# Performance work log

Measured on AMD Instinct MI355X. Metric: run time of the kernel, lower is better.

Reference implementation:

```python
import jax, jax.numpy as jnp
import numpy as np

B, N_ATOMS = 64, 127            # graphs, atoms per graph (uniform)
L = N_ATOMS + 1                 # +1 cls token
D_MODEL, NHEAD, NUM_LAYERS, D_FF = 1024, 16, 8, 3072
HEAD_DIM = D_MODEL // NHEAD
MAX_TOKENS = 131                # 121 + 10
NEIGH_VOCAB = 14 + 3            # max_neighbors + 3
DIST_VOCAB = 83 + 3             # max_distance + 3
EPS = 1e-5


def _dist_bins():
    # short_cutoff=0.9, long_cutoff=5.0, precision=0.05; first 3 edges overridden
    b = np.arange(0.9 - 3 * 0.05, 5.0, 0.05)
    b[:3] = [-1.0, 0.0, 0.01]
    return jnp.asarray(b, jnp.float32)  # len 85 -> digitize indices in [0, 85]


def _layer_norm(x, g, b):
    m = jnp.mean(x, -1, keepdims=True)
    v = jnp.var(x, -1, keepdims=True)
    return (x - m) * jax.lax.rsqrt(v + EPS) * g + b


def setup_inputs() -> dict:
    key = jax.random.key(0)
    ks = jax.random.split(key, 16)
    s = 0.02
    z = jax.random.randint(ks[0], (B * N_ATOMS,), 0, 119)
    hgs = jax.random.randint(ks[1], (B * N_ATOMS,), 0, 15)
    pos = jax.random.normal(ks[2], (B * N_ATOMS, 3), jnp.float32) * 3.0
    batch = jnp.repeat(jnp.arange(B, dtype=jnp.int64), N_ATOMS)
    atoms_emb = (jax.random.normal(ks[3], (MAX_TOKENS, D_MODEL), jnp.float32) * s).at[0].set(0.0)  # padding_idx=0
    neigh_emb = (jax.random.normal(ks[4], (NEIGH_VOCAB, D_MODEL), jnp.float32) * s).at[0].set(0.0)
    dist_emb = jax.random.normal(ks[5], (DIST_VOCAB, NHEAD), jnp.float32) * s  # row 0 forced to -inf in reference
    Wqkv = jax.random.normal(ks[6], (D_MODEL, 3 * D_MODEL), jnp.float32) * s
    bqkv = jnp.zeros((3 * D_MODEL,), jnp.float32)
    Wo = jax.random.normal(ks[7], (D_MODEL, D_MODEL), jnp.float32) * s
    bo = jnp.zeros((D_MODEL,), jnp.float32)
    W1 = jax.random.normal(ks[8], (D_MODEL, D_FF), jnp.float32) * s
    b1f = jnp.zeros((D_FF,), jnp.float32)
    W2 = jax.random.normal(ks[9], (D_FF, D_MODEL), jnp.float32) * s
    b2f = jnp.zeros((D_MODEL,), jnp.float32)
    ln1_g = jnp.ones((D_MODEL,), jnp.float32); ln1_b = jnp.zeros((D_MODEL,), jnp.float32)
    ln2_g = jnp.ones((D_MODEL,), jnp.float32); ln2_b = jnp.zeros((D_MODEL,), jnp.float32)
    return dict(z=z, hgs=hgs, pos=pos, batch=batch, atoms_emb=atoms_emb, neigh_emb=neigh_emb,
                dist_emb=dist_emb, Wqkv=Wqkv, bqkv=bqkv, Wo=Wo, bo=bo,
                W1=W1, b1f=b1f, W2=W2, b2f=b2f,
                ln1_g=ln1_g, ln1_b=ln1_b, ln2_g=ln2_g, ln2_b=ln2_b)


def reference(z, hgs, pos, batch, atoms_emb, neigh_emb, dist_emb,
              Wqkv, bqkv, Wo, bo, W1, b1f, W2, b2f, ln1_g, ln1_b, ln2_g, ln2_b):
    # batch is uniform (N_ATOMS per graph, sorted), so per-graph batching == reshape
    zb = z.reshape(B, N_ATOMS).astype(jnp.int32) + 2
    hb = hgs.reshape(B, N_ATOMS).astype(jnp.int32) + 2
    atoms = jnp.concatenate([jnp.ones((B, 1), jnp.int32), zb], axis=1)        # cls token = 1
    neighbors = jnp.concatenate([jnp.zeros((B, 1), jnp.int32), hb], axis=1)   # cls neighbors = 0

    p = pos.reshape(B, N_ATOMS, 3)
    dist = jnp.sqrt(jnp.sum((p[:, None, :, :] - p[:, :, None, :]) ** 2, axis=-1))  # (B,n,n)
    didx = jnp.digitize(dist, _dist_bins()).astype(jnp.int32)                      # self-loop -> 2
    distances = jnp.ones((B, L, L), jnp.int32).at[:, 1:, 1:].set(didx)             # cls row/col = 1

    # neg_inf_idx=0 padding mask row (unused here since no padding -> indices >= 1)
    w_d = dist_emb.at[0].set(-jnp.inf)
    d_mask = w_d[distances].transpose(0, 3, 1, 2)  # (B, H, L, L)

    x = atoms_emb[atoms] + neigh_emb[neighbors]    # (B, L, D)
    scale = 1.0 / jnp.sqrt(jnp.float32(HEAD_DIM))
    for _ in range(NUM_LAYERS):  # shared weights + shared attention bias
        qkv = x @ Wqkv + bqkv
        q, k, v = jnp.split(qkv, 3, axis=-1)
        q = q.reshape(B, L, NHEAD, HEAD_DIM)
        k = k.reshape(B, L, NHEAD, HEAD_DIM)
        v = v.reshape(B, L, NHEAD, HEAD_DIM)
        scores = jnp.einsum('blhd,bmhd->bhlm', q, k) * scale + d_mask
        a = jax.nn.softmax(scores, axis=-1)
        o = jnp.einsum('bhlm,bmhd->blhd', a, v).reshape(B, L, D_MODEL) @ Wo + bo
        x = _layer_norm(x + o, ln1_g, ln1_b)                      # post-norm (norm_first=False)
        h = jax.nn.gelu(x @ W1 + b1f, approximate=False) @ W2 + b2f
        x = _layer_norm(x + h, ln2_g, ln2_b)
    return x[:, 0]  # cls embedding, (B, D_MODEL)
```

## Files before the change

kernel.cpp:

```cpp
#include <hip/hip_runtime.h>
#include <cstdint>
#include <math.h>

typedef unsigned short u16;
typedef __attribute__((ext_vector_type(4))) float f32x4;
typedef __attribute__((ext_vector_type(8))) __bf16 bf16x8;
typedef __attribute__((ext_vector_type(8))) short short8;

typedef __attribute__((address_space(1))) void g_void;
typedef __attribute__((address_space(3))) void l_void;

__device__ __forceinline__ u16 f2bf(float f) {
  uint32_t u = __builtin_bit_cast(uint32_t, f);
  u += 0x7FFFu + ((u >> 16) & 1u);
  return (u16)(u >> 16);
}
__device__ __forceinline__ float bf2f(u16 h) {
  uint32_t u = ((uint32_t)h) << 16;
  return __builtin_bit_cast(float, u);
}

__device__ __forceinline__ void gload16(const void* g, void* l) {
  __builtin_amdgcn_global_load_lds((g_void*)g, (l_void*)l, 16, 0, 0);
}

__device__ __forceinline__ float gelu_exact(float x) {
  float a = x * 0.70710678118654752f;
  float s = fabsf(a);
  float t = __builtin_amdgcn_rcpf(fmaf(0.3275911f, s, 1.0f));
  float p = fmaf(fmaf(fmaf(fmaf(1.061405429f, t, -1.453152027f), t, 1.421413741f), t,
                      -0.284496736f), t, 0.254829592f);
  p *= t;
  float e = __expf(-s * s);
  float er = fmaf(-p, e, 1.0f);
  er = copysignf(er, a);
  return 0.5f * x * (1.0f + er);
}

__global__ void transpose_w(const float* __restrict__ W, u16* __restrict__ Wt, int K, int N) {
  __shared__ float t[32][33];
  const int nb = blockIdx.x * 32, kb = blockIdx.y * 32;
  const int tx = threadIdx.x, ty = threadIdx.y;
#pragma unroll
  for (int i = 0; i < 32; i += 8)
    t[ty + i][tx] = W[(size_t)(kb + ty + i) * N + nb + tx];
  __syncthreads();
#pragma unroll
  for (int i = 0; i < 32; i += 8)
    Wt[(size_t)(nb + ty + i) * K + kb + tx] = f2bf(t[tx][ty + i]);
}

__global__ void embed_k(const int* __restrict__ z, const int* __restrict__ hgs,
                        const float* __restrict__ ae, const float* __restrict__ ne,
                        u16* __restrict__ xb) {
  const int row = blockIdx.x;
  const int b = row >> 7, tl = row & 127;
  int ia = 1, in_ = 0;
  if (tl > 0) { ia = z[b * 127 + tl - 1] + 2; in_ = hgs[b * 127 + tl - 1] + 2; }
  const float* ar = ae + (size_t)ia * 1024;
  const float* nr = ne + (size_t)in_ * 1024;
  for (int c = threadIdx.x; c < 1024; c += 256)
    xb[(size_t)row * 1024 + c] = f2bf(ar[c] + nr[c]);
}

__global__ void mask_k(const float* __restrict__ pos, const float* __restrict__ demb,
                       u16* __restrict__ mask) {
  __shared__ float edges[85];
  __shared__ float dhT[16 * 86];
  const int blk = blockIdx.x;
  const int b = blk >> 7, lk = blk & 127;
  const int lq = threadIdx.x;
  if (lq < 85) {
    double e = 0.75 + 0.05 * (double)lq;
    float ef = (float)e;
    if (lq == 0) ef = -1.0f; else if (lq == 1) ef = 0.0f; else if (lq == 2) ef = 0.01f;
    edges[lq] = ef;
  }
  for (int i = lq; i < 16 * 86; i += 128) {
    const int h = i / 86, c = i - h * 86;
    float v = (c == 0) ? -INFINITY : demb[c * 16 + h] * 8.0f;
    dhT[i] = v;
  }
  __syncthreads();
  int c;
  if (lq == 0 || lk == 0) {
    c = 1;
  } else {
    const float* pi = pos + ((size_t)b * 127 + lq - 1) * 3;
    const float* pj = pos + ((size_t)b * 127 + lk - 1) * 3;
    const float dx = pi[0] - pj[0], dy = pi[1] - pj[1], dz = pi[2] - pj[2];
    const float d = sqrtf(dx * dx + dy * dy + dz * dz);
    int cnt = 0;
#pragma unroll
    for (int k2 = 0; k2 < 85; ++k2) cnt += (edges[k2] <= d) ? 1 : 0;
    c = cnt;
  }
#pragma unroll
  for (int h = 0; h < 16; ++h)
    mask[((size_t)(b * 16 + h) << 14) + lk * 128 + lq] = f2bf(dhT[h * 86 + c]);
}

template <int MODE>
__launch_bounds__(512, 4)
__global__ void gemmS(const u16* __restrict__ A, const u16* __restrict__ Bt,
                      const float* __restrict__ bias,
                      u16* __restrict__ O0, u16* __restrict__ O1, u16* __restrict__ O2,
                      int N, int K) {
  extern __shared__ char lds[];
  constexpr int SLAB = 24576;
  const int tid = threadIdx.x;
  const int w = tid >> 6, l = tid & 63;
  const int wr = w >> 1, wc = w & 1;
  const int nwg = gridDim.x;
  const int wg = (blockIdx.x & 7) * (nwg >> 3) + (blockIdx.x >> 3);
  const int ntn = N >> 7;
  const int bm = wg / ntn, bn = wg - (wg / ntn) * ntn;
  const int NT = K >> 5;

  const int colc = ((((l & 3) << 4) ^ (((l >> 2) & 8) << 2)) >> 1);
  const u16* Ag = A + (size_t)(bm * 256 + w * 16 + (l >> 2)) * K + colc;
  const u16* Bg = Bt + (size_t)(bn * 128 + w * 16 + (l >> 2)) * K + colc;
  const int ldst = w << 10;

  const int lo = ((l & 15) << 6) + (((l >> 4) << 4) ^ ((l & 8) << 2));

  f32x4 acc[4][4];
#pragma unroll
  for (int m = 0; m < 4; ++m)
#pragma unroll
    for (int n = 0; n < 4; ++n) acc[m][n] = f32x4{0.f, 0.f, 0.f, 0.f};

  char* p0 = lds;
  char* p1 = lds + SLAB;
  char* p2 = lds + 2 * SLAB;

  {
    gload16(Ag + 0, p0 + ldst);
    gload16(Ag + (size_t)128 * K + 0, p0 + 8192 + ldst);
    gload16(Bg + 0, p0 + 16384 + ldst);
    gload16(Ag + 32, p1 + ldst);
    gload16(Ag + (size_t)128 * K + 32, p1 + 8192 + ldst);
    gload16(Bg + 32, p1 + 16384 + ldst);
  }
  asm volatile("s_waitcnt vmcnt(3)" ::: "memory");
  __builtin_amdgcn_s_barrier();

  for (int t = 0; t < NT; ++t) {
    const bool pre = (t + 2 < NT);
    const int kb2 = (t + 2) << 5;
    const char* ab = p0 + (wr << 12);
    const char* bb = p0 + 16384 + (wc << 12);
    bf16x8 af[4], bf[4];
#pragma unroll
    for (int m = 0; m < 4; ++m) af[m] = *(const bf16x8*)(ab + (m << 10) + lo);
#pragma unroll
    for (int n = 0; n < 2; ++n) bf[n] = *(const bf16x8*)(bb + (n << 10) + lo);
    if (pre) {
      gload16(Ag + kb2, p2 + ldst);
      gload16(Ag + (size_t)128 * K + kb2, p2 + 8192 + ldst);
    }
    __builtin_amdgcn_s_barrier();
    asm volatile("s_waitcnt lgkmcnt(0)" ::: "memory");
    __builtin_amdgcn_s_setprio(1);
#pragma unroll
    for (int m = 0; m < 4; ++m)
#pragma unroll
      for (int n = 0; n < 2; ++n)
        acc[m][n] = __builtin_amdgcn_mfma_f32_16x16x32_bf16(af[m], bf[n], acc[m][n], 0, 0, 0);
    __builtin_amdgcn_s_setprio(0);
    __builtin_amdgcn_s_barrier();
#pragma unroll
    for (int n = 2; n < 4; ++n) bf[n] = *(const bf16x8*)(bb + (n << 10) + lo);
    if (pre) gload16(Bg + kb2, p2 + 16384 + ldst);
    __builtin_amdgcn_s_barrier();
    asm volatile("s_waitcnt lgkmcnt(0)" ::: "memory");
    __builtin_amdgcn_s_setprio(1);
#pragma unroll
    for (int m = 0; m < 4; ++m)
#pragma unroll
      for (int n = 2; n < 4; ++n)
        acc[m][n] = __builtin_amdgcn_mfma_f32_16x16x32_bf16(af[m], bf[n], acc[m][n], 0, 0, 0);
    __builtin_amdgcn_s_setprio(0);
    if (pre) asm volatile("s_waitcnt vmcnt(3)" ::: "memory");
    else     asm volatile("s_waitcnt vmcnt(0)" ::: "memory");
    __builtin_amdgcn_s_barrier();
    char* tmp = p0; p0 = p1; p1 = p2; p2 = tmp;
  }

  const int fr = l & 15, fq = l >> 4;
  const int colb = bn * 128 + wc * 64;
  const int rowb = bm * 256 + wr * 64;
  float bv[4];
#pragma unroll
  for (int n = 0; n < 4; ++n) bv[n] = bias[colb + n * 16 + fr];
  const int region = colb >> 10;

#pragma unroll
  for (int m = 0; m < 4; ++m) {
#pragma unroll
    for (int n = 0; n < 4; ++n) {
      const int col = colb + n * 16 + fr;
      if (MODE == 0 && region == 2) {
        const int row0_ = rowb + m * 16 + fq * 4;
        const int bI = row0_ >> 7, tl0 = row0_ & 127;
        const int c = col & 1023, h = c >> 6, d = c & 63;
        ushort4 pk;
        pk.x = f2bf(acc[m][n][0] + bv[n]);
        pk.y = f2bf(acc[m][n][1] + bv[n]);
        pk.z = f2bf(acc[m][n][2] + bv[n]);
        pk.w = f2bf(acc[m][n][3] + bv[n]);
        *(ushort4*)&O2[(((size_t)bI * 16 + h) * 64 + d) * 128 + tl0] = pk;
      } else {
#pragma unroll
        for (int j = 0; j < 4; ++j) {
          const int row = rowb + m * 16 + fq * 4 + j;
          float v = acc[m][n][j] + bv[n];
          if (MODE == 2) v = gelu_exact(v);
          if (MODE == 0) {
            const int bI = row >> 7, tl = row & 127;
            const int c = col & 1023, h = c >> 6, d = c & 63;
            if (region == 0) O0[(((size_t)bI * 16 + h) * 128 + tl) * 64 + d] = f2bf(v);
            else             O1[(((size_t)bI * 16 + h) * 128 + tl) * 64 + d] = f2bf(v);
          } else {
            O0[(size_t)row * N + col] = f2bf(v);
          }
        }
      }
    }
  }
}

__launch_bounds__(256, 2)
__global__ void gemm4r(const u16* __restrict__ A, const u16* __restrict__ Bt,
                       const float* __restrict__ bias, u16* __restrict__ O,
                       int N, int K) {
  extern __shared__ char lds[];
  const int tid = threadIdx.x;
  const int w = tid >> 6, l = tid & 63;
  const int wr = w >> 1, wc = w & 1;
  const int nwg = gridDim.x;
  const int wg = (blockIdx.x & 7) * (nwg >> 3) + (blockIdx.x >> 3);
  const int ntn = N >> 7;
  const int bm = wg / ntn, bn = wg - (wg / ntn) * ntn;
  const int NT = K >> 5;

  const int colc = ((((l & 3) << 4) ^ (((l >> 2) & 8) << 2)) >> 1);
  const u16* Ag = A + (size_t)(bm * 128 + w * 16 + (l >> 2)) * K + colc;
  const u16* Bg = Bt + (size_t)(bn * 128 + w * 16 + (l >> 2)) * K + colc;
  const int ldst = w << 10;

  auto stage = [&](int t) {
    char* buf = lds + ((t & 3) << 14);
    const int kb = t << 5;
    gload16(Ag + kb, buf + ldst);
    gload16(Ag + (size_t)64 * K + kb, buf + 4096 + ldst);
    gload16(Bg + kb, buf + 8192 + ldst);
    gload16(Bg + (size_t)64 * K + kb, buf + 12288 + ldst);
  };

  const int lo = ((l & 15) << 6) + (((l >> 4) << 4) ^ ((l & 8) << 2));

  f32x4 acc[4][4];
#pragma unroll
  for (int m = 0; m < 4; ++m)
#pragma unroll
    for (int n = 0; n < 4; ++n) acc[m][n] = f32x4{0.f, 0.f, 0.f, 0.f};

  auto compute = [&](int bi) {
    const char* ab = lds + (bi << 14) + (wr << 12);
    const char* bb = lds + (bi << 14) + 8192 + (wc << 12);
    bf16x8 af[4], bf[4];
#pragma unroll
    for (int m = 0; m < 4; ++m) af[m] = *(const bf16x8*)(ab + (m << 10) + lo);
#pragma unroll
    for (int n = 0; n < 4; ++n) bf[n] = *(const bf16x8*)(bb + (n << 10) + lo);
    __builtin_amdgcn_s_setprio(1);
#pragma unroll
    for (int m = 0; m < 4; ++m)
#pragma unroll
      for (int n = 0; n < 4; ++n)
        acc[m][n] = __builtin_amdgcn_mfma_f32_16x16x32_bf16(af[m], bf[n], acc[m][n], 0, 0, 0);
    __builtin_amdgcn_s_setprio(0);
  };

  stage(0); stage(1); stage(2);
  asm volatile("s_waitcnt vmcnt(8)" ::: "memory");
  __builtin_amdgcn_s_barrier();

  for (int t4 = 0; t4 + 4 < NT; t4 += 4) {
#pragma unroll
    for (int u = 0; u < 4; ++u) {
      stage(t4 + u + 3);
      compute(u);
      asm volatile("s_waitcnt vmcnt(8)" ::: "memory");
      __builtin_amdgcn_s_barrier();
    }
  }
  stage(NT - 1);
  compute(0);
  asm volatile("s_waitcnt vmcnt(8)" ::: "memory");
  __builtin_amdgcn_s_barrier();
  compute(1);
  asm volatile("s_waitcnt vmcnt(4)" ::: "memory");
  __builtin_amdgcn_s_barrier();
  compute(2);
  asm volatile("s_waitcnt vmcnt(0)" ::: "memory");
  __builtin_amdgcn_s_barrier();
  compute(3);

  const int fr = l & 15, fq = l >> 4;
  const int colb = bn * 128 + wc * 64;
  const int rowb = bm * 128 + wr * 64;
  float bv[4];
#pragma unroll
  for (int n = 0; n < 4; ++n) bv[n] = bias[colb + n * 16 + fr];
#pragma unroll
  for (int m = 0; m < 4; ++m)
#pragma unroll
    for (int n = 0; n < 4; ++n) {
      const int col = colb + n * 16 + fr;
#pragma unroll
      for (int j = 0; j < 4; ++j) {
        const int row = rowb + m * 16 + fq * 4 + j;
        O[(size_t)row * N + col] = f2bf(acc[m][n][j] + bv[n]);
      }
    }
}

__launch_bounds__(256)
__global__ void attn_kernel(const u16* __restrict__ Qg, const u16* __restrict__ Kg,
                            const u16* __restrict__ Vg,
                            const u16* __restrict__ mask,
                            u16* __restrict__ Og) {
  __shared__ u16 QK[2 * 128 * 64];
  __shared__ u16 Vt[64 * 128];
  const int tid = threadIdx.x;
  const int wv = tid >> 6;
  const int l = tid & 63;
  const int bh = blockIdx.x;
  const int b = bh >> 4;

  const char* Qs = (const char*)(Qg + (size_t)bh * 8192);
  const char* Ks = (const char*)(Kg + (size_t)bh * 8192);
  const char* Vs = (const char*)(Vg + (size_t)bh * 8192);
  char* QKb = (char*)QK;
  char* Vtb = (char*)Vt;
#pragma unroll
  for (int it = 0; it < 4; ++it) {
    const int r = it * 32 + (tid >> 3);
    const int cb = (tid & 7) * 16;
    const int sw = cb ^ ((r & 7) << 4);
    *(uint4*)(QKb + r * 128 + sw) = *(const uint4*)(Qs + r * 128 + cb);
    *(uint4*)(QKb + 16384 + r * 128 + sw) = *(const uint4*)(Ks + r * 128 + cb);
  }
#pragma unroll
  for (int it = 0; it < 4; ++it) {
    const int r = it * 16 + (tid >> 4);
    const int cb = (tid & 15) * 16;
    const int sw = cb ^ ((r & 7) << 4);
    *(uint4*)(Vtb + r * 256 + sw) = *(const uint4*)(Vs + r * 256 + cb);
  }

  const u16* m8 = mask + ((size_t)bh << 14);
  f32x4 s[2][8];
#pragma unroll
  for (int m = 0; m < 2; ++m) {
    const int r0 = wv * 32 + m * 16 + (l >> 4) * 4;
#pragma unroll
    for (int n = 0; n < 8; ++n) {
      const int col = n * 16 + (l & 15);
      const ushort4 mv = *(const ushort4*)(m8 + col * 128 + r0);
      s[m][n] = f32x4{bf2f(mv.x), bf2f(mv.y), bf2f(mv.z), bf2f(mv.w)};
    }
  }
  __syncthreads();

#pragma unroll
  for (int kk = 0; kk < 2; ++kk) {
    bf16x8 qa[2], kb[8];
#pragma unroll
    for (int m = 0; m < 2; ++m) {
      const int qr = wv * 32 + m * 16 + (l & 15);
      qa[m] = *(const bf16x8*)(QKb + qr * 128 + ((kk * 64 + (l >> 4) * 16) ^ ((qr & 7) << 4)));
    }
#pragma unroll
    for (int n = 0; n < 8; ++n) {
      const int kr = n * 16 + (l & 15);
      kb[n] = *(const bf16x8*)(QKb + 16384 + kr * 128 + ((kk * 64 + (l >> 4) * 16) ^ ((kr & 7) << 4)));
    }
#pragma unroll
    for (int m = 0; m < 2; ++m)
#pragma unroll
      for (int n = 0; n < 8; ++n)
        s[m][n] = __builtin_amdgcn_mfma_f32_16x16x32_bf16(qa[m], kb[n], s[m][n], 0, 0, 0);
  }

  float rinv[2][4];
#pragma unroll
  for (int m = 0; m < 2; ++m) {
#pragma unroll
    for (int j = 0; j < 4; ++j) {
      float vals[8];
#pragma unroll
      for (int n = 0; n < 8; ++n)
        vals[n] = s[m][n][j] * 0.125f;
      float mx = vals[0];
#pragma unroll
      for (int n = 1; n < 8; ++n) mx = fmaxf(mx, vals[n]);
#pragma unroll
      for (int o = 1; o < 16; o <<= 1) mx = fmaxf(mx, __shfl_xor(mx, o, 64));
      float sum = 0.f;
#pragma unroll
      for (int n = 0; n < 8; ++n) { vals[n] = expf(vals[n] - mx); sum += vals[n]; }
#pragma unroll
      for (int o = 1; o < 16; o <<= 1) sum += __shfl_xor(sum, o, 64);
      rinv[m][j] = 1.f / sum;
#pragma unroll
      for (int n = 0; n < 8; ++n) s[m][n][j] = vals[n];
    }
  }
  __syncthreads();
  char* Pb = QKb + wv * 8192;
#pragma unroll
  for (int m = 0; m < 2; ++m)
#pragma unroll
    for (int n = 0; n < 8; ++n)
#pragma unroll
      for (int j = 0; j < 4; ++j) {
        const int pr = m * 16 + (l >> 4) * 4 + j;
        const int pc = (n * 16 + (l & 15)) * 2;
        *(u16*)(Pb + pr * 256 + (pc ^ ((pr & 7) << 4))) = f2bf(s[m][n][j]);
      }

  f32x4 o_[2][4];
#pragma unroll
  for (int m = 0; m < 2; ++m)
#pragma unroll
    for (int n = 0; n < 4; ++n) o_[m][n] = f32x4{0.f, 0.f, 0.f, 0.f};
#pragma unroll
  for (int ks = 0; ks < 4; ++ks) {
    bf16x8 pa[2], vb[4];
#pragma unroll
    for (int m = 0; m < 2; ++m) {
      const int pr = m * 16 + (l & 15);
      pa[m] = *(const bf16x8*)(Pb + pr * 256 + ((ks * 64 + (l >> 4) * 16) ^ ((pr & 7) << 4)));
    }
#pragma unroll
    for (int n = 0; n < 4; ++n) {
      const int vr = n * 16 + (l & 15);
      vb[n] = *(const bf16x8*)(Vtb + vr * 256 + ((ks * 64 + (l >> 4) * 16) ^ ((vr & 7) << 4)));
    }
#pragma unroll
    for (int m = 0; m < 2; ++m)
#pragma unroll
      for (int n = 0; n < 4; ++n)
        o_[m][n] = __builtin_amdgcn_mfma_f32_16x16x32_bf16(pa[m], vb[n], o_[m][n], 0, 0, 0);
  }
  const int h = bh & 15;
#pragma unroll
  for (int m = 0; m < 2; ++m)
#pragma unroll
    for (int n = 0; n < 4; ++n)
#pragma unroll
      for (int j = 0; j < 4; ++j) {
        const int lo2 = wv * 32 + m * 16 + (l >> 4) * 4 + j;
        const int d = n * 16 + (l & 15);
        Og[((size_t)b * 128 + lo2) * 1024 + h * 64 + d] = f2bf(o_[m][n][j] * rinv[m][j]);
      }
}

__launch_bounds__(256)
__global__ void ln_res(u16* __restrict__ xb, const u16* __restrict__ o,
                       const float* __restrict__ gam, const float* __restrict__ bet,
                       float* __restrict__ cls_out) {
  const int row = blockIdx.x * 4 + (threadIdx.x >> 6);
  const int l = threadIdx.x & 63;
  const size_t base = (size_t)row * 1024 + l * 16;
  const int c0 = l * 16;
  float v[16], gv[16], bb[16];
  const short8 xa = *(const short8*)(xb + base);
  const short8 xc = *(const short8*)(xb + base + 8);
  const short8 oa = *(const short8*)(o + base);
  const short8 oc = *(const short8*)(o + base + 8);
#pragma unroll
  for (int i = 0; i < 4; ++i) {
    *(float4*)&gv[i * 4] = *(const float4*)(gam + c0 + i * 4);
    *(float4*)&bb[i * 4] = *(const float4*)(bet + c0 + i * 4);
  }
  float s = 0.f, sq = 0.f;
#pragma unroll
  for (int i = 0; i < 8; ++i) {
    v[i] = bf2f((u16)xa[i]) + bf2f((u16)oa[i]);
    v[i + 8] = bf2f((u16)xc[i]) + bf2f((u16)oc[i]);
  }
#pragma unroll
  for (int i = 0; i < 16; ++i) { s += v[i]; sq += v[i] * v[i]; }
#pragma unroll
  for (int off = 1; off < 64; off <<= 1) {
    s += __shfl_xor(s, off, 64);
    sq += __shfl_xor(sq, off, 64);
  }
  const float mean = s * (1.f / 1024.f);
  const float var = sq * (1.f / 1024.f) - mean * mean;
  const float rstd = rsqrtf(var + 1e-5f);
  short8 ra, rc;
#pragma unroll
  for (int i = 0; i < 8; ++i) {
    const float ya = (v[i] - mean) * rstd * gv[i] + bb[i];
    const float yc = (v[i + 8] - mean) * rstd * gv[i + 8] + bb[i + 8];
    ra[i] = (short)f2bf(ya);
    rc[i] = (short)f2bf(yc);
    if ((row & 127) == 0) {
      cls_out[(size_t)(row >> 7) * 1024 + c0 + i] = ya;
      cls_out[(size_t)(row >> 7) * 1024 + c0 + 8 + i] = yc;
    }
  }
  *(short8*)(xb + base) = ra;
  *(short8*)(xb + base + 8) = rc;
}

extern "C" void kernel_launch(void* const* d_in, const int* in_sizes, int n_in,
                              void* d_out, int out_size, void* d_ws, size_t ws_size,
                              hipStream_t stream) {
  const int* z = (const int*)d_in[0];
  const int* hgs = (const int*)d_in[1];
  const float* pos = (const float*)d_in[2];
  const float* atoms_emb = (const float*)d_in[4];
  const float* neigh_emb = (const float*)d_in[5];
  const float* dist_emb = (const float*)d_in[6];
  const float* Wqkv = (const float*)d_in[7];
  const float* bqkv = (const float*)d_in[8];
  const float* Wo = (const float*)d_in[9];
  const float* bo = (const float*)d_in[10];
  const float* W1 = (const float*)d_in[11];
  const float* b1f = (const float*)d_in[12];
  const float* W2 = (const float*)d_in[13];
  const float* b2f = (const float*)d_in[14];
  const float* ln1g = (const float*)d_in[15];
  const float* ln1b = (const float*)d_in[16];
  const float* ln2g = (const float*)d_in[17];
  const float* ln2b = (const float*)d_in[18];

  size_t off = 0;
  char* wsb = (char*)d_ws;
  auto alc = [&](size_t bytes) { void* p = wsb + off; off += (bytes + 255) & ~(size_t)255; return p; };
  u16* xb = (u16*)alc(8192ull * 1024 * 2);
  u16* q = (u16*)alc(8192ull * 1024 * 2);
  u16* k = (u16*)alc(8192ull * 1024 * 2);
  u16* v = (u16*)alc(8192ull * 1024 * 2);
  u16* proj = (u16*)alc(8192ull * 1024 * 2);
  u16* big = (u16*)alc(8192ull * 3072 * 2);
  u16* wqkvt = (u16*)alc(3072ull * 1024 * 2);
  u16* wot = (u16*)alc(1024ull * 1024 * 2);
  u16* w1t = (u16*)alc(3072ull * 1024 * 2);
  u16* w2t = (u16*)alc(1024ull * 3072 * 2);
  u16* mask = (u16*)alc(64ull * 16 * 128 * 128 * 2);

  hipFuncSetAttribute((const void*)gemmS<0>, hipFuncAttributeMaxDynamicSharedMemorySize, 73728);
  hipFuncSetAttribute((const void*)gemmS<2>, hipFuncAttributeMaxDynamicSharedMemorySize, 73728);
  hipFuncSetAttribute((const void*)gemm4r, hipFuncAttributeMaxDynamicSharedMemorySize, 65536);

  transpose_w<<<dim3(96, 32), dim3(32, 8), 0, stream>>>(Wqkv, wqkvt, 1024, 3072);
  transpose_w<<<dim3(32, 32), dim3(32, 8), 0, stream>>>(Wo, wot, 1024, 1024);
  transpose_w<<<dim3(96, 32), dim3(32, 8), 0, stream>>>(W1, w1t, 1024, 3072);
  transpose_w<<<dim3(32, 96), dim3(32, 8), 0, stream>>>(W2, w2t, 3072, 1024);
  embed_k<<<8192, 256, 0, stream>>>(z, hgs, atoms_emb, neigh_emb, xb);
  mask_k<<<8192, 128, 0, stream>>>(pos, dist_emb, mask);

  float* cls = (float*)d_out;
  for (int layer = 0; layer < 8; ++layer) {
    gemmS<0><<<768, 512, 73728, stream>>>(xb, wqkvt, bqkv, q, k, v, 3072, 1024);
    attn_kernel<<<1024, 256, 0, stream>>>(q, k, v, mask, big);
    gemm4r<<<512, 256, 65536, stream>>>(big, wot, bo, proj, 1024, 1024);
    ln_res<<<2048, 256, 0, stream>>>(xb, proj, ln1g, ln1b, cls);
    gemmS<2><<<768, 512, 73728, stream>>>(xb, w1t, b1f, big, nullptr, nullptr, 3072, 1024);
    gemm4r<<<512, 256, 65536, stream>>>(big, w2t, b2f, proj, 1024, 3072);
    ln_res<<<2048, 256, 0, stream>>>(xb, proj, ln2g, ln2b, cls);
  }
}
```

Measured before the change: 2.190 ms.

## Double-buffer GEMM register fragments to overlap LDS reads with MFMA

Splits the GEMM inner step into a fragment-read phase and an MFMA phase. It keeps two sets of A/B register fragments so the next tile's LDS reads are issued while the current tile's MFMAs run. The main loop is rewritten to advance two k-tiles per iteration, and the wait thresholds are tightened to vmcnt(4)/vmcnt(0). The aim is to hide LDS read latency behind matrix math. In exchange it uses more registers, leaves fewer global loads in flight, and assumes the k-tile count is even.

```diff
diff --git a/kernel.cpp b/kernel.cpp
--- a/kernel.cpp
+++ b/kernel.cpp
@@ -260,20 +260,22 @@
 
   const int lo = ((l & 15) << 6) + (((l >> 4) << 4) ^ ((l & 8) << 2));
 
-  f32x4 acc[4][4];
-#pragma unroll
-  for (int m = 0; m < 4; ++m)
-#pragma unroll
-    for (int n = 0; n < 4; ++n) acc[m][n] = f32x4{0.f, 0.f, 0.f, 0.f};
-
-  auto compute = [&](int bi) {
+  auto readfr = [&](int bi, bf16x8* af, bf16x8* bf) {
     const char* ab = lds + (bi << 14) + (wr << 12);
     const char* bb = lds + (bi << 14) + 8192 + (wc << 12);
-    bf16x8 af[4], bf[4];
 #pragma unroll
     for (int m = 0; m < 4; ++m) af[m] = *(const bf16x8*)(ab + (m << 10) + lo);
 #pragma unroll
     for (int n = 0; n < 4; ++n) bf[n] = *(const bf16x8*)(bb + (n << 10) + lo);
+  };
+
+  f32x4 acc[4][4];
+#pragma unroll
+  for (int m = 0; m < 4; ++m)
+#pragma unroll
+    for (int n = 0; n < 4; ++n) acc[m][n] = f32x4{0.f, 0.f, 0.f, 0.f};
+
+  auto mm = [&](bf16x8* af, bf16x8* bf) {
     __builtin_amdgcn_s_setprio(1);
 #pragma unroll
     for (int m = 0; m < 4; ++m)
@@ -284,29 +286,26 @@
   };
 
   stage(0); stage(1); stage(2);
-  asm volatile("s_waitcnt vmcnt(8)" ::: "memory");
-  __builtin_amdgcn_s_barrier();
-
-  for (int t4 = 0; t4 + 4 < NT; t4 += 4) {
-#pragma unroll
-    for (int u = 0; u < 4; ++u) {
-      stage(t4 + u + 3);
-      compute(u);
-      asm volatile("s_waitcnt vmcnt(8)" ::: "memory");
-      __builtin_amdgcn_s_barrier();
-    }
-  }
-  stage(NT - 1);
-  compute(0);
-  asm volatile("s_waitcnt vmcnt(8)" ::: "memory");
-  __builtin_amdgcn_s_barrier();
-  compute(1);
   asm volatile("s_waitcnt vmcnt(4)" ::: "memory");
   __builtin_amdgcn_s_barrier();
-  compute(2);
-  asm volatile("s_waitcnt vmcnt(0)" ::: "memory");
-  __builtin_amdgcn_s_barrier();
-  compute(3);
+
+  bf16x8 afA[4], bfA[4], afB[4], bfB[4];
+  readfr(0, afA, bfA);
+
+  for (int t = 0; t < NT; t += 2) {
+    if (t + 3 < NT) stage(t + 3);
+    mm(afA, bfA);
+    readfr((t + 1) & 3, afB, bfB);
+    if (t + 3 < NT) asm volatile("s_waitcnt vmcnt(4)" ::: "memory");
+    else            asm volatile("s_waitcnt vmcnt(0)" ::: "memory");
+    __builtin_amdgcn_s_barrier();
+    if (t + 4 < NT) stage(t + 4);
+    mm(afB, bfB);
+    if (t + 2 < NT) readfr((t + 2) & 3, afA, bfA);
+    if (t + 4 < NT) asm volatile("s_waitcnt vmcnt(4)" ::: "memory");
+    else            asm volatile("s_waitcnt vmcnt(0)" ::: "memory");
+    __builtin_amdgcn_s_barrier();
+  }
 
   const int fr = l & 15, fq = l >> 4;
   const int colb = bn * 128 + wc * 64;
```

Result: no change. 2.213 ms (+1.1%).

## Enlarge QKV/FFN1 GEMM tile to 256x256 with 64-wide K double buffering

Applied to the files above, without the earlier changes.

Replaces the 256x128 triple-buffered GEMM with a 256x256 tile where each of 8 waves computes 128x64 (8x4 MFMA accumulators), processing K in 64-wide steps with double-buffered 128KB LDS. This raises arithmetic intensity per LDS/global load and halves the grid to 384 blocks. In exchange it uses more registers and LDS, which limits occupancy to roughly one block per CU. A grid of 384 blocks on 256 CUs also leaves an uneven final wave.

```diff
diff --git a/kernel.cpp b/kernel.cpp
--- a/kernel.cpp
+++ b/kernel.cpp
@@ -101,102 +101,137 @@
 }
 
 template <int MODE>
-__launch_bounds__(512, 4)
-__global__ void gemmS(const u16* __restrict__ A, const u16* __restrict__ Bt,
-                      const float* __restrict__ bias,
-                      u16* __restrict__ O0, u16* __restrict__ O1, u16* __restrict__ O2,
-                      int N, int K) {
+__launch_bounds__(512, 2)
+__global__ void gemm8p(const u16* __restrict__ A, const u16* __restrict__ Bt,
+                       const float* __restrict__ bias,
+                       u16* __restrict__ O0, u16* __restrict__ O1, u16* __restrict__ O2,
+                       int N, int K) {
   extern __shared__ char lds[];
-  constexpr int SLAB = 24576;
   const int tid = threadIdx.x;
   const int w = tid >> 6, l = tid & 63;
-  const int wr = w >> 1, wc = w & 1;
+  const int wr = w >> 2, wc = w & 3;
   const int nwg = gridDim.x;
   const int wg = (blockIdx.x & 7) * (nwg >> 3) + (blockIdx.x >> 3);
-  const int ntn = N >> 7;
+  const int ntn = N >> 8;
   const int bm = wg / ntn, bn = wg - (wg / ntn) * ntn;
-  const int NT = K >> 5;
+  const int NT = K >> 6;
 
   const int colc = ((((l & 3) << 4) ^ (((l >> 2) & 8) << 2)) >> 1);
   const u16* Ag = A + (size_t)(bm * 256 + w * 16 + (l >> 2)) * K + colc;
-  const u16* Bg = Bt + (size_t)(bn * 128 + w * 16 + (l >> 2)) * K + colc;
+  const u16* Bg = Bt + (size_t)(bn * 256 + w * 16 + (l >> 2)) * K + colc;
   const int ldst = w << 10;
 
+  auto slab = [&](int op, int buf, int kk) -> char* {
+    return lds + op * 65536 + (((buf << 1) | kk) << 14);
+  };
+  auto stA = [&](int t, int kk) {
+    char* s = slab(0, t & 1, kk);
+    const int kb = t * 64 + kk * 32;
+    gload16(Ag + kb, s + ldst);
+    gload16(Ag + (size_t)128 * K + kb, s + 8192 + ldst);
+  };
+  auto stB = [&](int t, int kk) {
+    char* s = slab(1, t & 1, kk);
+    const int kb = t * 64 + kk * 32;
+    gload16(Bg + kb, s + ldst);
+    gload16(Bg + (size_t)128 * K + kb, s + 8192 + ldst);
+  };
+
   const int lo = ((l & 15) << 6) + (((l >> 4) << 4) ^ ((l & 8) << 2));
 
-  f32x4 acc[4][4];
-#pragma unroll
-  for (int m = 0; m < 4; ++m)
+  f32x4 acc[8][4];
+#pragma unroll
+  for (int m = 0; m < 8; ++m)
 #pragma unroll
     for (int n = 0; n < 4; ++n) acc[m][n] = f32x4{0.f, 0.f, 0.f, 0.f};
 
-  char* p0 = lds;
-  char* p1 = lds + SLAB;
-  char* p2 = lds + 2 * SLAB;
-
-  {
-    gload16(Ag + 0, p0 + ldst);
-    gload16(Ag + (size_t)128 * K + 0, p0 + 8192 + ldst);
-    gload16(Bg + 0, p0 + 16384 + ldst);
-    gload16(Ag + 32, p1 + ldst);
-    gload16(Ag + (size_t)128 * K + 32, p1 + 8192 + ldst);
-    gload16(Bg + 32, p1 + 16384 + ldst);
-  }
-  asm volatile("s_waitcnt vmcnt(3)" ::: "memory");
+  stA(0, 0); stB(0, 0); stA(0, 1); stB(0, 1);
+  asm volatile("s_waitcnt vmcnt(0)" ::: "memory");
   __builtin_amdgcn_s_barrier();
 
   for (int t = 0; t < NT; ++t) {
-    const bool pre = (t + 2 < NT);
-    const int kb2 = (t + 2) << 5;
-    const char* ab = p0 + (wr << 12);
-    const char* bb = p0 + 16384 + (wc << 12);
+    const int p = t & 1;
+    const bool pre = (t + 1 < NT);
+    const char* sa0 = slab(0, p, 0) + (wr << 13);
+    const char* sa1 = slab(0, p, 1) + (wr << 13);
+    const char* sb0 = slab(1, p, 0) + (wc << 12);
+    const char* sb1 = slab(1, p, 1) + (wc << 12);
     bf16x8 af[4], bf[4];
-#pragma unroll
-    for (int m = 0; m < 4; ++m) af[m] = *(const bf16x8*)(ab + (m << 10) + lo);
-#pragma unroll
-    for (int n = 0; n < 2; ++n) bf[n] = *(const bf16x8*)(bb + (n << 10) + lo);
-    if (pre) {
-      gload16(Ag + kb2, p2 + ldst);
-      gload16(Ag + (size_t)128 * K + kb2, p2 + 8192 + ldst);
-    }
+
+    asm volatile("s_waitcnt vmcnt(4)" ::: "memory");
+#pragma unroll
+    for (int m = 0; m < 4; ++m) af[m] = *(const bf16x8*)(sa0 + (m << 10) + lo);
+#pragma unroll
+    for (int n = 0; n < 4; ++n) bf[n] = *(const bf16x8*)(sb0 + (n << 10) + lo);
+    if (pre) stA(t + 1, 0);
     __builtin_amdgcn_s_barrier();
     asm volatile("s_waitcnt lgkmcnt(0)" ::: "memory");
     __builtin_amdgcn_s_setprio(1);
 #pragma unroll
     for (int m = 0; m < 4; ++m)
 #pragma unroll
-      for (int n = 0; n < 2; ++n)
+      for (int n = 0; n < 4; ++n)
         acc[m][n] = __builtin_amdgcn_mfma_f32_16x16x32_bf16(af[m], bf[n], acc[m][n], 0, 0, 0);
     __builtin_amdgcn_s_setprio(0);
     __builtin_amdgcn_s_barrier();
-#pragma unroll
-    for (int n = 2; n < 4; ++n) bf[n] = *(const bf16x8*)(bb + (n << 10) + lo);
-    if (pre) gload16(Bg + kb2, p2 + 16384 + ldst);
+
+#pragma unroll
+    for (int m = 0; m < 4; ++m) af[m] = *(const bf16x8*)(sa0 + ((m + 4) << 10) + lo);
+    if (pre) stB(t + 1, 0);
     __builtin_amdgcn_s_barrier();
     asm volatile("s_waitcnt lgkmcnt(0)" ::: "memory");
     __builtin_amdgcn_s_setprio(1);
 #pragma unroll
     for (int m = 0; m < 4; ++m)
 #pragma unroll
-      for (int n = 2; n < 4; ++n)
+      for (int n = 0; n < 4; ++n)
+        acc[m + 4][n] = __builtin_amdgcn_mfma_f32_16x16x32_bf16(af[m], bf[n], acc[m + 4][n], 0, 0, 0);
+    __builtin_amdgcn_s_setprio(0);
+    __builtin_amdgcn_s_barrier();
+
+    if (pre) asm volatile("s_waitcnt vmcnt(4)" ::: "memory");
+    else     asm volatile("s_waitcnt vmcnt(0)" ::: "memory");
+#pragma unroll
+    for (int m = 0; m < 4; ++m) af[m] = *(const bf16x8*)(sa1 + (m << 10) + lo);
+#pragma unroll
+    for (int n = 0; n < 4; ++n) bf[n] = *(const bf16x8*)(sb1 + (n << 10) + lo);
+    if (pre) stA(t + 1, 1);
+    __builtin_amdgcn_s_barrier();
+    asm volatile("s_waitcnt lgkmcnt(0)" ::: "memory");
+    __builtin_amdgcn_s_setprio(1);
+#pragma unroll
+    for (int m = 0; m < 4; ++m)
+#pragma unroll
+      for (int n = 0; n < 4; ++n)
         acc[m][n] = __builtin_amdgcn_mfma_f32_16x16x32_bf16(af[m], bf[n], acc[m][n], 0, 0, 0);
     __builtin_amdgcn_s_setprio(0);
-    if (pre) asm volatile("s_waitcnt vmcnt(3)" ::: "memory");
-    else     asm volatile("s_waitcnt vmcnt(0)" ::: "memory");
-    __builtin_amdgcn_s_barrier();
-    char* tmp = p0; p0 = p1; p1 = p2; p2 = tmp;
+    __builtin_amdgcn_s_barrier();
+
+#pragma unroll
+    for (int m = 0; m < 4; ++m) af[m] = *(const bf16x8*)(sa1 + ((m + 4) << 10) + lo);
+    if (pre) stB(t + 1, 1);
+    __builtin_amdgcn_s_barrier();
+    asm volatile("s_waitcnt lgkmcnt(0)" ::: "memory");
+    __builtin_amdgcn_s_setprio(1);
+#pragma unroll
+    for (int m = 0; m < 4; ++m)
+#pragma unroll
+      for (int n = 0; n < 4; ++n)
+        acc[m + 4][n] = __builtin_amdgcn_mfma_f32_16x16x32_bf16(af[m], bf[n], acc[m + 4][n], 0, 0, 0);
+    __builtin_amdgcn_s_setprio(0);
+    __builtin_amdgcn_s_barrier();
   }
 
   const int fr = l & 15, fq = l >> 4;
-  const int colb = bn * 128 + wc * 64;
-  const int rowb = bm * 256 + wr * 64;
+  const int colb = bn * 256 + wc * 64;
+  const int rowb = bm * 256 + wr * 128;
   float bv[4];
 #pragma unroll
   for (int n = 0; n < 4; ++n) bv[n] = bias[colb + n * 16 + fr];
   const int region = colb >> 10;
 
 #pragma unroll
-  for (int m = 0; m < 4; ++m) {
+  for (int m = 0; m < 8; ++m) {
 #pragma unroll
     for (int n = 0; n < 4; ++n) {
       const int col = colb + n * 16 + fr;
@@ -556,8 +591,8 @@
   u16* w2t = (u16*)alc(1024ull * 3072 * 2);
   u16* mask = (u16*)alc(64ull * 16 * 128 * 128 * 2);
 
-  hipFuncSetAttribute((const void*)gemmS<0>, hipFuncAttributeMaxDynamicSharedMemorySize, 73728);
-  hipFuncSetAttribute((const void*)gemmS<2>, hipFuncAttributeMaxDynamicSharedMemorySize, 73728);
+  hipFuncSetAttribute((const void*)gemm8p<0>, hipFuncAttributeMaxDynamicSharedMemorySize, 131072);
+  hipFuncSetAttribute((const void*)gemm8p<2>, hipFuncAttributeMaxDynamicSharedMemorySize, 131072);
   hipFuncSetAttribute((const void*)gemm4r, hipFuncAttributeMaxDynamicSharedMemorySize, 65536);
 
   transpose_w<<<dim3(96, 32), dim3(32, 8), 0, stream>>>(Wqkv, wqkvt, 1024, 3072);
@@ -569,11 +604,11 @@
 
   float* cls = (float*)d_out;
   for (int layer = 0; layer < 8; ++layer) {
-    gemmS<0><<<768, 512, 73728, stream>>>(xb, wqkvt, bqkv, q, k, v, 3072, 1024);
+    gemm8p<0><<<384, 512, 131072, stream>>>(xb, wqkvt, bqkv, q, k, v, 3072, 1024);
     attn_kernel<<<1024, 256, 0, stream>>>(q, k, v, mask, big);
     gemm4r<<<512, 256, 65536, stream>>>(big, wot, bo, proj, 1024, 1024);
     ln_res<<<2048, 256, 0, stream>>>(xb, proj, ln1g, ln1b, cls);
-    gemmS<2><<<768, 512, 73728, stream>>>(xb, w1t, b1f, big, nullptr, nullptr, 3072, 1024);
+    gemm8p<2><<<384, 512, 131072, stream>>>(xb, w1t, b1f, big, nullptr, nullptr, 3072, 1024);
     gemm4r<<<512, 256, 65536, stream>>>(big, w2t, b2f, proj, 1024, 3072);
     ln_res<<<2048, 256, 0, stream>>>(xb, proj, ln2g, ln2b, cls);
   }
```

After: 2.372 ms. +8.3%, slower.
